# Kernel tuning notes

Measured on AMD Instinct MI355X. Metric: run time of the kernel, lower is better.

Reference implementation:

```python
import jax, jax.numpy as jnp
import numpy as np

M, K, N, G = 8192, 4096, 11008, 128  # tokens, in_features, out_features, quant groups (group_size=32)


def setup_inputs() -> dict:
    key = jax.random.key(0)
    k1, k2, k3, k4 = jax.random.split(key, 4)
    A = jax.random.normal(k1, (M, K), dtype=jnp.float32)
    # packed int4 weights: two nibbles per uint8 byte along K
    weight = jax.random.randint(k2, (K // 2, N), 0, 256, dtype=jnp.int32).astype(jnp.uint8)
    # per-group, per-output-channel dequant scales (positive, small)
    weight_scale = jax.random.uniform(k3, (G, N), dtype=jnp.float32, minval=0.005, maxval=0.02)
    bias = jax.random.normal(k4, (N,), dtype=jnp.float32) * 0.01
    return {"A": A, "weight": weight, "weight_scale": weight_scale, "bias": bias}


def unpack_int4(x, x_scale):
    # x: uint8 [K//2, N]; x_scale: float [G, N] -> float [K, N]
    Kd = x.shape[0] * 2
    Gd, Nd = x_scale.shape
    group_k = Kd // Gd
    # row 2i = low nibble, row 2i+1 = high nibble (matches shifts [0, 4])
    nib = jnp.stack([x & 15, (x >> 4) & 15], axis=1).reshape(Kd, Nd)
    w = (nib.astype(jnp.int8) - 8).astype(x_scale.dtype)
    return (w.reshape(Gd, group_k, Nd) * x_scale[:, None, :]).reshape(Kd, Nd)


def reference(A, weight, weight_scale, bias):
    # out = A @ dequant(weight) + bias
    W = unpack_int4(weight, weight_scale)
    return A @ W + bias
```

## Files before the change

kernel.cpp:

```cpp
#include <hip/hip_runtime.h>
#include <hip/hip_bf16.h>
#include <stdint.h>

typedef __attribute__((ext_vector_type(8))) short bf16x8;
typedef __attribute__((ext_vector_type(4))) float f32x4;
typedef __attribute__((ext_vector_type(4))) int i32x4;

constexpr int Mdim = 8192;
constexpr int Ndim = 11008;
constexpr int Kdim = 4096;
constexpr int NT = Kdim / 64;
constexpr int NMF = Mdim / 16;
constexpr int NWG = (Mdim / 256) * (Ndim / 128);
constexpr int CPX = NWG / 8;
constexpr int NBN = Ndim / 128;

__device__ __forceinline__ unsigned short f2bf(float f) {
    __bf16 h = (__bf16)f;
    return __builtin_bit_cast(unsigned short, h);
}

__global__ __launch_bounds__(256) void prepAS_kernel(const float* __restrict__ A,
                                                     char* __restrict__ Af,
                                                     float* __restrict__ sA,
                                                     const float* __restrict__ Ws,
                                                     float* __restrict__ Fc,
                                                     float* __restrict__ sCol)
{
    const int tid = threadIdx.x;
    if (blockIdx.x >= NMF) {
        const int n = ((int)blockIdx.x - NMF) * 256 + tid;
        float mx = 0.f;
        for (int g = 0; g < 128; ++g) mx = fmaxf(mx, Ws[(size_t)g * Ndim + n]);
        Fc[n]   = 15.875f / mx;
        sCol[n] = mx * (8.0f / 127.0f);
        return;
    }
    __shared__ float sm[16][17];
    const int g = blockIdx.x;
    const int r   = tid >> 4;
    const int seg = tid & 15;
    const float* rowp = A + (size_t)(16 * g + r) * Kdim + seg * 256;
    float m = 0.f;
#pragma unroll 8
    for (int j = 0; j < 64; ++j) {
        const f32x4 v = *(const f32x4*)(rowp + j * 4);
#pragma unroll
        for (int e = 0; e < 4; ++e) m = fmaxf(m, fabsf(v[e]));
    }
    sm[r][seg] = m;
    __syncthreads();
    if (seg == 0) {
        float mo = 0.f;
#pragma unroll
        for (int i = 0; i < 16; ++i) mo = fmaxf(mo, sm[r][i]);
        sA[16 * g + r] = fmaxf(mo, 1e-20f) * (1.0f / 127.0f);
    }
    const int row = tid & 15;
    float mr = 0.f;
#pragma unroll
    for (int i = 0; i < 16; ++i) mr = fmaxf(mr, sm[row][i]);
    const float inv = 127.0f / fmaxf(mr, 1e-20f);
    const int l  = tid & 63;
    const int q  = tid >> 6;
    const int ch = l >> 4;
    const float* src0 = A + (size_t)(16 * g + row) * Kdim + ch * 16;
    char* dst0 = Af + (size_t)g * 65536 + (size_t)tid * 16;
#pragma unroll 4
    for (int it = 0; it < 16; ++it) {
        const int kt = it * 4 + q;
        const float* s = src0 + kt * 64;
        char o[16];
#pragma unroll
        for (int jj = 0; jj < 4; ++jj) {
            const f32x4 v = *(const f32x4*)(s + jj * 4);
#pragma unroll
            for (int e = 0; e < 4; ++e) o[jj * 4 + e] = (char)__float2int_rn(v[e] * inv);
        }
        *(i32x4*)(dst0 + it * 4096) = *(const i32x4*)o;
    }
}

__global__ __launch_bounds__(256) void wq_kernel(const int* __restrict__ Wq,
                                                 const float* __restrict__ Ws,
                                                 const float* __restrict__ Fc,
                                                 char* __restrict__ Wf)
{
    __shared__ char T[64][80];
    const int kt = blockIdx.x % (Kdim / 64);
    const int nt = blockIdx.x / (Kdim / 64);
    const int k0 = kt * 64, n0 = nt * 64;
    const int t = threadIdx.x;

    const int pr   = t >> 3;
    const int nloc = (t & 7) * 8;
    const int* wp = Wq + (size_t)(k0 / 2 + pr) * Ndim + n0 + nloc;
    const i32x4 ra = *(const i32x4*)wp;
    const i32x4 rb = *(const i32x4*)(wp + 4);
    const int g = (k0 + 2 * pr) >> 5;
    const float* sp = Ws + (size_t)g * Ndim + n0 + nloc;
    const f32x4 s0 = *(const f32x4*)sp;
    const f32x4 s1 = *(const f32x4*)(sp + 4);
    const f32x4 f0 = *(const f32x4*)(Fc + n0 + nloc);
    const f32x4 f1 = *(const f32x4*)(Fc + n0 + nloc + 4);
#pragma unroll
    for (int i = 0; i < 8; ++i) {
        const int v = (i < 4) ? ra[i] : rb[i - 4];
        const float sf = ((i < 4) ? s0[i] : s1[i - 4]) * ((i < 4) ? f0[i] : f1[i - 4]);
        T[nloc + i][2 * pr]     = (char)__float2int_rn((float)((v & 15) - 8) * sf);
        T[nloc + i][2 * pr + 1] = (char)__float2int_rn((float)(((v >> 4) & 15) - 8) * sf);
    }
    __syncthreads();
    const int nl = t >> 2;
    const int ko = (t & 3) * 16;
    const i32x4 o = *(const i32x4*)&T[nl][ko];
    const int nf  = n0 / 16 + (nl >> 4);
    const int row = nl & 15;
    const int ch  = t & 3;
    *(i32x4*)(Wf + ((size_t)nf * 64 + kt) * 1024 + ch * 256 + row * 16) = o;
}

__global__ __launch_bounds__(256, 2) void gemm_i8_flat(
    const char* __restrict__ Af,
    const char* __restrict__ Wf,
    const float* __restrict__ sA,
    const float* __restrict__ sCol,
    const float* __restrict__ Bias,
    float* __restrict__ Out)
{
    const int tid  = threadIdx.x;
    const int lane = tid & 63;
    const int wid  = tid >> 6;
    const int wr   = wid >> 1;
    const int wc   = wid & 1;
    const int l15  = lane & 15;
    const int l4   = lane >> 4;

    const int wg  = ((int)blockIdx.x % 8) * CPX + (int)blockIdx.x / 8;
    const int bm = wg / NBN, bn = wg % NBN;
    const int m0 = bm * 256, n0 = bn * 128;

    const char* aBase = Af + ((size_t)(m0 / 16 + wr * 8) * 64) * 1024 + lane * 16;
    const char* bBase = Wf + ((size_t)(n0 / 16 + wc * 4) * 64) * 1024 + lane * 16;

#define LOADT(T, AV, BV)                                                      \
    {                                                                         \
        _Pragma("unroll")                                                     \
        for (int fm = 0; fm < 8; ++fm)                                        \
            AV[fm] = *(const i32x4*)(aBase + fm * 65536 + (T) * 1024);        \
        _Pragma("unroll")                                                     \
        for (int fn = 0; fn < 4; ++fn)                                        \
            BV[fn] = *(const i32x4*)(bBase + fn * 65536 + (T) * 1024);        \
    }

    i32x4 acc[8][4];
#pragma unroll
    for (int i = 0; i < 8; ++i)
#pragma unroll
        for (int j = 0; j < 4; ++j) acc[i][j] = (i32x4){0, 0, 0, 0};

    i32x4 aP[8], bP[4], aQ[8], bQ[4];
    LOADT(0, aP, bP);

#define TILE(T, CA, CB, NA, NB)                                               \
    {                                                                         \
        if ((T) + 1 < NT) LOADT((T) + 1, NA, NB);                             \
        __builtin_amdgcn_s_setprio(1);                                        \
        _Pragma("unroll")                                                     \
        for (int fm = 0; fm < 8; ++fm) {                                      \
            _Pragma("unroll")                                                 \
            for (int fn = 0; fn < 4; ++fn)                                    \
                acc[fm][fn] = __builtin_amdgcn_mfma_i32_16x16x64_i8(          \
                    CA[fm], CB[fn], acc[fm][fn], 0, 0, 0);                    \
        }                                                                     \
        __builtin_amdgcn_s_setprio(0);                                        \
    }

    for (int t2 = 0; t2 < NT; t2 += 2) {
        TILE(t2,     aP, bP, aQ, bQ);
        TILE(t2 + 1, aQ, bQ, aP, bP);
    }
#undef LOADT
#undef TILE

    const int rb = l4 * 4;
    float sc[4], bb[4];
#pragma unroll
    for (int fn = 0; fn < 4; ++fn) {
        const int ng = n0 + wc * 64 + fn * 16 + l15;
        sc[fn] = sCol[ng];
        bb[fn] = Bias[ng];
    }
#pragma unroll
    for (int fm = 0; fm < 8; ++fm) {
        const size_t mg = (size_t)(m0 + wr * 128 + fm * 16 + rb);
#pragma unroll
        for (int r = 0; r < 4; ++r) {
            const float sa = sA[mg + r];
#pragma unroll
            for (int fn = 0; fn < 4; ++fn) {
                const int ng = n0 + wc * 64 + fn * 16 + l15;
                __builtin_nontemporal_store((float)acc[fm][fn][r] * sa * sc[fn] + bb[fn],
                                            &Out[(mg + r) * Ndim + ng]);
            }
        }
    }
}

constexpr int SA = 72;
__global__ __launch_bounds__(256) void w4a32_fused_kernel(
    const float* __restrict__ A,
    const int* __restrict__ Wq,
    const float* __restrict__ Ws,
    const float* __restrict__ Bias,
    float* __restrict__ Out)
{
    __shared__ unsigned short As[128 * SA];
    __shared__ unsigned short Bs[128 * SA];
    const int tid = threadIdx.x;
    const int nbn = Ndim / 128;
    const int bn = blockIdx.x % nbn;
    const int bm = blockIdx.x / nbn;
    const int m0 = bm * 128, n0 = bn * 128;
    const int lane = tid & 63;
    const int wid  = tid >> 6;
    const int wr   = wid >> 1;
    const int wc   = wid & 1;
    const int l15  = lane & 15;
    const int l4   = lane >> 4;
    f32x4 acc[4][4];
#pragma unroll
    for (int i = 0; i < 4; ++i)
#pragma unroll
        for (int j = 0; j < 4; ++j) acc[i][j] = (f32x4){0.f, 0.f, 0.f, 0.f};
    const int a_tr = tid >> 3;
    const int a_tc = (tid & 7) * 8;
    const int kp2  = tid >> 4;
    const int n8   = (tid & 15) * 8;
    for (int kt = 0; kt < Kdim / 64; ++kt) {
        const int k0 = kt * 64;
        __syncthreads();
#pragma unroll
        for (int j = 0; j < 4; ++j) {
            const int ml = a_tr + 32 * j;
            const float* src = A + (size_t)(m0 + ml) * Kdim + (k0 + a_tc);
            const f32x4 x0 = *(const f32x4*)src;
            const f32x4 x1 = *(const f32x4*)(src + 4);
            union { bf16x8 v; unsigned short u[8]; } h;
            h.u[0] = f2bf(x0[0]); h.u[1] = f2bf(x0[1]);
            h.u[2] = f2bf(x0[2]); h.u[3] = f2bf(x0[3]);
            h.u[4] = f2bf(x1[0]); h.u[5] = f2bf(x1[1]);
            h.u[6] = f2bf(x1[2]); h.u[7] = f2bf(x1[3]);
            *(bf16x8*)(&As[ml * SA + (a_tc ^ ((ml & 7) << 3))]) = h.v;
        }
        {
            const int pr = kt * 32 + 2 * kp2;
            const int* wp = Wq + (size_t)pr * Ndim + (n0 + n8);
            const i32x4 r0a = *(const i32x4*)wp;
            const i32x4 r0b = *(const i32x4*)(wp + 4);
            const i32x4 r1a = *(const i32x4*)(wp + Ndim);
            const i32x4 r1b = *(const i32x4*)(wp + Ndim + 4);
            const int g = 2 * kt + (kp2 >> 3);
            const float* sp = Ws + (size_t)g * Ndim + (n0 + n8);
            const f32x4 s0 = *(const f32x4*)sp;
            const f32x4 s1 = *(const f32x4*)(sp + 4);
#pragma unroll
            for (int i = 0; i < 8; ++i) {
                const float s = (i < 4) ? s0[i] : s1[i - 4];
                const int b0 = (i < 4) ? r0a[i] : r0b[i - 4];
                const int b1 = (i < 4) ? r1a[i] : r1b[i - 4];
                union { unsigned long long v; unsigned short u[4]; } o;
                o.u[0] = f2bf((float)((b0 & 15) - 8) * s);
                o.u[1] = f2bf((float)(((b0 >> 4) & 15) - 8) * s);
                o.u[2] = f2bf((float)((b1 & 15) - 8) * s);
                o.u[3] = f2bf((float)(((b1 >> 4) & 15) - 8) * s);
                const int nl = n8 + i;
                const int swzz = ((nl ^ (nl >> 3)) & 7) << 3;
                *(unsigned long long*)(&Bs[nl * SA + ((4 * kp2) ^ swzz)]) = o.v;
            }
        }
        __syncthreads();
#pragma unroll
        for (int ks = 0; ks < 2; ++ks) {
            const int kb  = ks * 32 + l4 * 8;
            const int swa = (l15 & 7) << 3;
            bf16x8 af[4], bfr[4];
#pragma unroll
            for (int fm = 0; fm < 4; ++fm) {
                const int row = wr * 64 + fm * 16 + l15;
                af[fm] = *(const bf16x8*)(&As[row * SA + (kb ^ swa)]);
            }
#pragma unroll
            for (int fn = 0; fn < 4; ++fn) {
                const int nrow = wc * 64 + fn * 16 + l15;
                const int swb = ((nrow ^ (nrow >> 3)) & 7) << 3;
                bfr[fn] = *(const bf16x8*)(&Bs[nrow * SA + (kb ^ swb)]);
            }
#pragma unroll
            for (int fm = 0; fm < 4; ++fm)
#pragma unroll
                for (int fn = 0; fn < 4; ++fn)
                    acc[fm][fn] = __builtin_amdgcn_mfma_f32_16x16x32_bf16(
                        af[fm], bfr[fn], acc[fm][fn], 0, 0, 0);
        }
    }
    const int rb = l4 * 4;
    float bv[4];
#pragma unroll
    for (int fn = 0; fn < 4; ++fn)
        bv[fn] = Bias[n0 + wc * 64 + fn * 16 + l15];
#pragma unroll
    for (int fm = 0; fm < 4; ++fm) {
        const size_t mg = (size_t)(m0 + wr * 64 + fm * 16 + rb);
#pragma unroll
        for (int fn = 0; fn < 4; ++fn) {
            const int ng = n0 + wc * 64 + fn * 16 + l15;
            const float b = bv[fn];
#pragma unroll
            for (int r = 0; r < 4; ++r)
                Out[(mg + r) * Ndim + ng] = acc[fm][fn][r] + b;
        }
    }
}

extern "C" void kernel_launch(void* const* d_in, const int* in_sizes, int n_in,
                              void* d_out, int out_size, void* d_ws, size_t ws_size,
                              hipStream_t stream) {
    const float* A    = (const float*)d_in[0];
    const int* Wq     = (const int*)d_in[1];
    const float* Ws   = (const float*)d_in[2];
    const float* Bias = (const float*)d_in[3];
    float* Out        = (float*)d_out;

    const size_t offAf = 0;
    const size_t offWf = (size_t)Mdim * Kdim;
    const size_t offSA = offWf + (size_t)Ndim / 16 * 16 * Kdim;
    const size_t offF  = offSA + (size_t)Mdim * 4;
    const size_t offSC = offF + (size_t)Ndim * 4;
    const size_t need  = offSC + (size_t)Ndim * 4;

    if (ws_size >= need) {
        char*  Af   = (char*)d_ws + offAf;
        char*  Wf   = (char*)d_ws + offWf;
        float* sAp  = (float*)((char*)d_ws + offSA);
        float* Fc   = (float*)((char*)d_ws + offF);
        float* sCol = (float*)((char*)d_ws + offSC);
        prepAS_kernel<<<NMF + Ndim / 256, 256, 0, stream>>>(A, Af, sAp, Ws, Fc, sCol);
        wq_kernel<<<(Kdim / 64) * (Ndim / 64), 256, 0, stream>>>(Wq, Ws, Fc, Wf);
        gemm_i8_flat<<<NWG, 256, 0, stream>>>(Af, Wf, sAp, sCol, Bias, Out);
    } else {
        w4a32_fused_kernel<<<(Mdim / 128) * (Ndim / 128), 256, 0, stream>>>(A, Wq, Ws, Bias, Out);
    }
}
```

Before: 493.3 us.

## Stage A tiles through LDS with async global_load_lds triple buffering

```diff
diff --git a/kernel.cpp b/kernel.cpp
--- a/kernel.cpp
+++ b/kernel.cpp
@@ -18,6 +18,13 @@
 __device__ __forceinline__ unsigned short f2bf(float f) {
     __bf16 h = (__bf16)f;
     return __builtin_bit_cast(unsigned short, h);
+}
+
+__device__ __forceinline__ void gload16(const void* g, void* lds) {
+    __builtin_amdgcn_global_load_lds(
+        (const __attribute__((address_space(1))) unsigned int*)g,
+        (__attribute__((address_space(3))) unsigned int*)lds,
+        16, 0, 0);
 }
 
 __global__ __launch_bounds__(256) void prepAS_kernel(const float* __restrict__ A,
@@ -120,7 +127,7 @@
     *(i32x4*)(Wf + ((size_t)nf * 64 + kt) * 1024 + ch * 256 + row * 16) = o;
 }
 
-__global__ __launch_bounds__(256, 2) void gemm_i8_flat(
+__global__ __launch_bounds__(256, 2) void gemm_i8_hyb(
     const char* __restrict__ Af,
     const char* __restrict__ Wf,
     const float* __restrict__ sA,
@@ -128,6 +135,8 @@
     const float* __restrict__ Bias,
     float* __restrict__ Out)
 {
+    __shared__ char sh[49152];
+
     const int tid  = threadIdx.x;
     const int lane = tid & 63;
     const int wid  = tid >> 6;
@@ -140,14 +149,17 @@
     const int bm = wg / NBN, bn = wg % NBN;
     const int m0 = bm * 256, n0 = bn * 128;
 
-    const char* aBase = Af + ((size_t)(m0 / 16 + wr * 8) * 64) * 1024 + lane * 16;
-    const char* bBase = Wf + ((size_t)(n0 / 16 + wc * 4) * 64) * 1024 + lane * 16;
-
-#define LOADT(T, AV, BV)                                                      \
+    const char* aDmaSrc = Af + ((size_t)(m0 / 16 + wid) * 64) * 1024 + (lane << 4);
+    auto stageA = [&](int tt) {
+        char* base = &sh[(tt % 3) * 16384 + tid * 16];
+#pragma unroll
+        for (int j = 0; j < 4; ++j)
+            gload16(aDmaSrc + (size_t)(4 * j) * 65536 + tt * 1024, base + j * 4096);
+    };
+
+    const char* bBase = Wf + ((size_t)(n0 / 16 + wc * 4) * 64) * 1024 + (lane << 4);
+#define LOADB(T, BV)                                                          \
     {                                                                         \
-        _Pragma("unroll")                                                     \
-        for (int fm = 0; fm < 8; ++fm)                                        \
-            AV[fm] = *(const i32x4*)(aBase + fm * 65536 + (T) * 1024);        \
         _Pragma("unroll")                                                     \
         for (int fn = 0; fn < 4; ++fn)                                        \
             BV[fn] = *(const i32x4*)(bBase + fn * 65536 + (T) * 1024);        \
@@ -159,28 +171,80 @@
 #pragma unroll
         for (int j = 0; j < 4; ++j) acc[i][j] = (i32x4){0, 0, 0, 0};
 
-    i32x4 aP[8], bP[4], aQ[8], bQ[4];
-    LOADT(0, aP, bP);
-
-#define TILE(T, CA, CB, NA, NB)                                               \
+    i32x4 bP[4], bQ[4];
+    stageA(0);
+    stageA(1);
+    LOADB(0, bP);
+    asm volatile("s_waitcnt vmcnt(8)" ::: "memory");
+    __builtin_amdgcn_s_barrier();
+
+#define TILE(T, CB, NB)                                                       \
     {                                                                         \
-        if ((T) + 1 < NT) LOADT((T) + 1, NA, NB);                             \
+        const char* aslot = &sh[((T) % 3) * 16384 + (wr * 8) * 1024 + (lane << 4)]; \
+        i32x4 av[8];                                                          \
+        _Pragma("unroll")                                                     \
+        for (int fm = 0; fm < 8; ++fm)                                        \
+            av[fm] = *(const i32x4*)(aslot + fm * 1024);                      \
+        if ((T) + 2 < NT) stageA((T) + 2);                                    \
+        if ((T) + 1 < NT) LOADB((T) + 1, NB);                                 \
         __builtin_amdgcn_s_setprio(1);                                        \
         _Pragma("unroll")                                                     \
         for (int fm = 0; fm < 8; ++fm) {                                      \
             _Pragma("unroll")                                                 \
             for (int fn = 0; fn < 4; ++fn)                                    \
                 acc[fm][fn] = __builtin_amdgcn_mfma_i32_16x16x64_i8(          \
-                    CA[fm], CB[fn], acc[fm][fn], 0, 0, 0);                    \
+                    CB##_a[fm], CB[fn], acc[fm][fn], 0, 0, 0);                \
         }                                                                     \
         __builtin_amdgcn_s_setprio(0);                                        \
     }
 
     for (int t2 = 0; t2 < NT; t2 += 2) {
-        TILE(t2,     aP, bP, aQ, bQ);
-        TILE(t2 + 1, aQ, bQ, aP, bP);
-    }
-#undef LOADT
+        {
+            const int T = t2;
+            const char* aslot = &sh[(T % 3) * 16384 + (wr * 8) * 1024 + (lane << 4)];
+            i32x4 av[8];
+#pragma unroll
+            for (int fm = 0; fm < 8; ++fm)
+                av[fm] = *(const i32x4*)(aslot + fm * 1024);
+            if (T + 2 < NT) stageA(T + 2);
+            if (T + 1 < NT) LOADB(T + 1, bQ);
+            __builtin_amdgcn_s_setprio(1);
+#pragma unroll
+            for (int fm = 0; fm < 8; ++fm)
+#pragma unroll
+                for (int fn = 0; fn < 4; ++fn)
+                    acc[fm][fn] = __builtin_amdgcn_mfma_i32_16x16x64_i8(
+                        av[fm], bP[fn], acc[fm][fn], 0, 0, 0);
+            __builtin_amdgcn_s_setprio(0);
+            if (T < NT - 2)       asm volatile("s_waitcnt vmcnt(8)" ::: "memory");
+            else if (T == NT - 2) asm volatile("s_waitcnt vmcnt(0)" ::: "memory");
+            asm volatile("" ::: "memory");
+            __builtin_amdgcn_s_barrier();
+        }
+        {
+            const int T = t2 + 1;
+            const char* aslot = &sh[(T % 3) * 16384 + (wr * 8) * 1024 + (lane << 4)];
+            i32x4 av[8];
+#pragma unroll
+            for (int fm = 0; fm < 8; ++fm)
+                av[fm] = *(const i32x4*)(aslot + fm * 1024);
+            if (T + 2 < NT) stageA(T + 2);
+            if (T + 1 < NT) LOADB(T + 1, bP);
+            __builtin_amdgcn_s_setprio(1);
+#pragma unroll
+            for (int fm = 0; fm < 8; ++fm)
+#pragma unroll
+                for (int fn = 0; fn < 4; ++fn)
+                    acc[fm][fn] = __builtin_amdgcn_mfma_i32_16x16x64_i8(
+                        av[fm], bQ[fn], acc[fm][fn], 0, 0, 0);
+            __builtin_amdgcn_s_setprio(0);
+            if (T < NT - 2)       asm volatile("s_waitcnt vmcnt(8)" ::: "memory");
+            else if (T == NT - 2) asm volatile("s_waitcnt vmcnt(0)" ::: "memory");
+            asm volatile("" ::: "memory");
+            __builtin_amdgcn_s_barrier();
+        }
+    }
+#undef LOADB
 #undef TILE
 
     const int rb = l4 * 4;
@@ -334,7 +398,7 @@
 
     const size_t offAf = 0;
     const size_t offWf = (size_t)Mdim * Kdim;
-    const size_t offSA = offWf + (size_t)Ndim / 16 * 16 * Kdim;
+    const size_t offSA = offWf + (size_t)Ndim * Kdim;
     const size_t offF  = offSA + (size_t)Mdim * 4;
     const size_t offSC = offF + (size_t)Ndim * 4;
     const size_t need  = offSC + (size_t)Ndim * 4;
@@ -347,7 +411,7 @@
         float* sCol = (float*)((char*)d_ws + offSC);
         prepAS_kernel<<<NMF + Ndim / 256, 256, 0, stream>>>(A, Af, sAp, Ws, Fc, sCol);
         wq_kernel<<<(Kdim / 64) * (Ndim / 64), 256, 0, stream>>>(Wq, Ws, Fc, Wf);
-        gemm_i8_flat<<<NWG, 256, 0, stream>>>(Af, Wf, sAp, sCol, Bias, Out);
+        gemm_i8_hyb<<<NWG, 256, 0, stream>>>(Af, Wf, sAp, sCol, Bias, Out);
     } else {
         w4a32_fused_kernel<<<(Mdim / 128) * (Ndim / 128), 256, 0, stream>>>(A, Wq, Ws, Bias, Out);
     }
```

Result: faster. 483.6 us (-2.0%).
